# Performance work log

Measured on AMD Instinct MI355X. Metric: run time of the kernel, lower is better.

## Reference

```python
import jax, jax.numpy as jnp
import numpy as np

IN_DIM, OUT_DIM = 256, 64
ALPHA = 0.2  # leaky relu negative slope
NEG_INF = -1e30


def setup_inputs() -> dict:
    key = jax.random.key(0)
    k1, k2, k3, k4 = jax.random.split(key, 4)
    B, N = 8, 2048
    h = jax.random.normal(k1, (B, N, IN_DIM), dtype=jnp.float32)
    adj = jax.random.randint(k2, (B, N, N), 0, 2, dtype=jnp.int32)
    # ensure no fully-isolated node (avoids softmax over all -inf)
    idx = jnp.arange(N)
    adj = adj.at[:, idx, idx].set(1)
    # params: fc.weight [out,in] -> store transposed [in,out]; attn_fc.weight [1, 2*out] -> [2*out]
    W = jax.random.normal(k3, (IN_DIM, OUT_DIM), dtype=jnp.float32) / np.sqrt(IN_DIM)
    a = jax.random.normal(k4, (2 * OUT_DIM,), dtype=jnp.float32) / np.sqrt(2 * OUT_DIM)
    return {"h": h, "adj": adj, "W": W, "a": a}


def reference(h, adj, W, a):
    # Wh: [B,N,D]
    Wh = jnp.einsum("bni,io->bno", h, W)
    D = Wh.shape[-1]
    # concat-based additive attention decomposed: e[b,i,j] = lrelu(a1.Wh_i + a2.Wh_j)
    a1, a2 = a[:D], a[D:]
    s1 = Wh @ a1  # [B,N] contribution of row node i
    s2 = Wh @ a2  # [B,N] contribution of col node j
    e = jax.nn.leaky_relu(s1[:, :, None] + s2[:, None, :], negative_slope=ALPHA)  # [B,N,N]
    e = jnp.where(adj == 0, NEG_INF, e)
    attn = jax.nn.softmax(e, axis=-1)
    # dropout is identity in eval mode
    return jnp.einsum("bij,bjd->bid", attn, Wh)
```

## Files before the change

kernel.cpp:

```cpp
#include <hip/hip_runtime.h>
#include <math.h>

#define NB 8
#define NN 2048
#define IN_DIM 256
#define OUT_DIM 64
#define ALPHA 0.2f
#define JSPLIT 4

typedef __attribute__((ext_vector_type(8))) short bf16x8;
typedef __attribute__((ext_vector_type(4))) float f32x4;
typedef __attribute__((ext_vector_type(4))) int   i32x4;

__device__ __forceinline__ unsigned short f2bf(float x) {
    union { float f; unsigned u; } v; v.f = x;
    unsigned r = v.u + 0x7FFF + ((v.u >> 16) & 1);
    return (unsigned short)(r >> 16);
}

#define WT_STRIDE 264
__global__ __launch_bounds__(256) void wh_kernel(const float* __restrict__ h,
                                                 const float* __restrict__ W,
                                                 const float* __restrict__ a,
                                                 unsigned short* __restrict__ Whbt,
                                                 float* __restrict__ s1,
                                                 float* __restrict__ s2) {
    __shared__ unsigned short Wt[OUT_DIM * WT_STRIDE];
    const int t = threadIdx.x;

    #pragma unroll 8
    for (int rep = 0; rep < 64; ++rep) {
        const int id = rep * 256 + t;
        const int k = id >> 6, n = id & 63;
        Wt[n * WT_STRIDE + k] = f2bf(W[id]);
    }
    __syncthreads();

    const int lane = t & 63, wv = t >> 6;
    const int m = lane & 15, quad = lane >> 4;
    const long gr0 = (long)(blockIdx.x * 4 + wv) * 16;

    f32x4 acc[4];
    #pragma unroll
    for (int nt = 0; nt < 4; ++nt) acc[nt] = (f32x4){0.f, 0.f, 0.f, 0.f};

    #pragma unroll
    for (int ks = 0; ks < 8; ++ks) {
        const int k0 = ks * 32;
        const float* hp = h + (gr0 + m) * IN_DIM + k0 + quad * 8;
        const float4 ha = *(const float4*)hp;
        const float4 hb = *(const float4*)(hp + 4);
        bf16x8 af;
        af[0] = (short)f2bf(ha.x); af[1] = (short)f2bf(ha.y);
        af[2] = (short)f2bf(ha.z); af[3] = (short)f2bf(ha.w);
        af[4] = (short)f2bf(hb.x); af[5] = (short)f2bf(hb.y);
        af[6] = (short)f2bf(hb.z); af[7] = (short)f2bf(hb.w);
        #pragma unroll
        for (int nt = 0; nt < 4; ++nt) {
            const bf16x8 bf_ = *(const bf16x8*)(const void*)
                &Wt[(nt * 16 + m) * WT_STRIDE + k0 + quad * 8];
            acc[nt] = __builtin_amdgcn_mfma_f32_16x16x32_bf16(af, bf_, acc[nt], 0, 0, 0);
        }
    }

    const int b  = (int)(gr0 >> 11);
    const int ib = (int)(gr0 & 2047);

    #pragma unroll
    for (int nt = 0; nt < 4; ++nt) {
        ushort4 w4;
        w4.x = f2bf(acc[nt][0]); w4.y = f2bf(acc[nt][1]);
        w4.z = f2bf(acc[nt][2]); w4.w = f2bf(acc[nt][3]);
        *(ushort4*)&Whbt[((long)(b * OUT_DIM + nt * 16 + m) << 11) + ib + quad * 4] = w4;
    }

    float a1v[4], a2v[4];
    #pragma unroll
    for (int nt = 0; nt < 4; ++nt) {
        a1v[nt] = a[nt * 16 + m];
        a2v[nt] = a[OUT_DIM + nt * 16 + m];
    }
    #pragma unroll
    for (int reg = 0; reg < 4; ++reg) {
        float p1 = 0.f, p2 = 0.f;
        #pragma unroll
        for (int nt = 0; nt < 4; ++nt) {
            p1 += acc[nt][reg] * a1v[nt];
            p2 += acc[nt][reg] * a2v[nt];
        }
        #pragma unroll
        for (int off = 1; off < 16; off <<= 1) {
            p1 += __shfl_xor(p1, off, 64);
            p2 += __shfl_xor(p2, off, 64);
        }
        if (m == 0) {
            s1[gr0 + quad * 4 + reg] = p1;
            s2[gr0 + quad * 4 + reg] = p2;
        }
    }
}

__device__ __forceinline__ float pcalc(int av, float s2e, float s1v) {
    float e = s1v + s2e;
    e = e > 0.f ? e : ALPHA * e;
    const float p = __expf(e);
    return av != 0 ? p : 0.f;
}

__global__ __launch_bounds__(256, 4) void attn_kernel(const int* __restrict__ adj,
                                                      const unsigned short* __restrict__ Whbt,
                                                      const float* __restrict__ s1,
                                                      const float* __restrict__ s2,
                                                      float* __restrict__ part,
                                                      float* __restrict__ lpart) {
    const int t = threadIdx.x, lane = t & 63, wv = t >> 6;
    const int bid = blockIdx.x;
    const int js  = bid & (JSPLIT - 1);
    const int itg = (bid >> 2) & 31;
    const int b   = bid >> 7;
    const int i0  = itg * 64 + wv * 16;
    const int jlo = js * (NN / JSPLIT);

    const int m = lane & 15, quad = lane >> 4;

    const int*   adjp = adj + (long)b * NN * NN + (long)(i0 + m) * NN + jlo + quad * 8;
    const float* s2p  = s2 + b * NN + jlo + quad * 8;
    const unsigned short* wbase = Whbt + ((long)(b * OUT_DIM) << 11) + jlo + quad * 8;
    const float s1v = s1[b * NN + i0 + m];

    f32x4 acc[4];
    #pragma unroll
    for (int nt = 0; nt < 4; ++nt) acc[nt] = (f32x4){0.f, 0.f, 0.f, 0.f};
    f32x4 racc = (f32x4){0.f, 0.f, 0.f, 0.f};

    bf16x8 bones;
    #pragma unroll
    for (int e = 0; e < 8; ++e) bones[e] = (short)0x3F80;

    i32x4  av0[2], av1[2];
    float4 sv0[2], sv1[2];
    #pragma unroll
    for (int p = 0; p < 2; ++p) {
        av0[p] = __builtin_nontemporal_load((const i32x4*)(adjp + p * 32));
        av1[p] = __builtin_nontemporal_load((const i32x4*)(adjp + p * 32 + 4));
        sv0[p] = *(const float4*)(s2p + p * 32);
        sv1[p] = *(const float4*)(s2p + p * 32 + 4);
    }

    #pragma unroll 2
    for (int ks = 0; ks < 16; ++ks) {
        const int j0 = ks * 32;
        const int cur = ks & 1;

        bf16x8 bfr[4];
        #pragma unroll
        for (int nt = 0; nt < 4; ++nt)
            bfr[nt] = *(const bf16x8*)(const void*)
                &wbase[(((long)(nt * 16 + m)) << 11) + j0];

        const i32x4  ca0 = av0[cur], ca1 = av1[cur];
        const float4 cs0 = sv0[cur], cs1 = sv1[cur];
        if (ks < 14) {
            av0[cur] = __builtin_nontemporal_load((const i32x4*)(adjp + j0 + 64));
            av1[cur] = __builtin_nontemporal_load((const i32x4*)(adjp + j0 + 68));
            sv0[cur] = *(const float4*)(s2p + j0 + 64);
            sv1[cur] = *(const float4*)(s2p + j0 + 68);
        }

        float pv[8];
        pv[0] = pcalc(ca0.x, cs0.x, s1v); pv[1] = pcalc(ca0.y, cs0.y, s1v);
        pv[2] = pcalc(ca0.z, cs0.z, s1v); pv[3] = pcalc(ca0.w, cs0.w, s1v);
        pv[4] = pcalc(ca1.x, cs1.x, s1v); pv[5] = pcalc(ca1.y, cs1.y, s1v);
        pv[6] = pcalc(ca1.z, cs1.z, s1v); pv[7] = pcalc(ca1.w, cs1.w, s1v);

        bf16x8 af;
        #pragma unroll
        for (int e = 0; e < 8; ++e) af[e] = (short)f2bf(pv[e]);

        #pragma unroll
        for (int nt = 0; nt < 4; ++nt)
            acc[nt] = __builtin_amdgcn_mfma_f32_16x16x32_bf16(af, bfr[nt], acc[nt], 0, 0, 0);
        racc = __builtin_amdgcn_mfma_f32_16x16x32_bf16(af, bones, racc, 0, 0, 0);
    }

    if (m == 0) {
        #pragma unroll
        for (int reg = 0; reg < 4; ++reg)
            lpart[js * (NB * NN) + b * NN + i0 + quad * 4 + reg] = racc[reg];
    }

    float* pp = part + (long)js * ((long)NB * NN * OUT_DIM)
                     + ((long)(b * NN + i0) << 6);
    #pragma unroll
    for (int nt = 0; nt < 4; ++nt)
        #pragma unroll
        for (int reg = 0; reg < 4; ++reg)
            pp[(quad * 4 + reg) * OUT_DIM + nt * 16 + m] = acc[nt][reg];
}

__global__ __launch_bounds__(256) void finalize_kernel(const float* __restrict__ part,
                                                       const float* __restrict__ lpart,
                                                       float* __restrict__ out) {
    const int idx = blockIdx.x * 256 + threadIdx.x;
    const int row = idx >> 4;
    float l = 0.f;
    #pragma unroll
    for (int s = 0; s < JSPLIT; ++s) l += lpart[s * (NB * NN) + row];
    float4 v = make_float4(0.f, 0.f, 0.f, 0.f);
    const float4* p4 = (const float4*)part;
    #pragma unroll
    for (int s = 0; s < JSPLIT; ++s) {
        const float4 p = p4[(long)s * ((long)NB * NN * OUT_DIM / 4) + idx];
        v.x += p.x; v.y += p.y; v.z += p.z; v.w += p.w;
    }
    const float inv = 1.f / l;
    v.x *= inv; v.y *= inv; v.z *= inv; v.w *= inv;
    ((float4*)out)[idx] = v;
}

extern "C" void kernel_launch(void* const* d_in, const int* in_sizes, int n_in,
                              void* d_out, int out_size, void* d_ws, size_t ws_size,
                              hipStream_t stream) {
    const float* h   = (const float*)d_in[0];
    const int*   adj = (const int*)d_in[1];
    const float* W   = (const float*)d_in[2];
    const float* a   = (const float*)d_in[3];
    float* out = (float*)d_out;

    float* s1    = (float*)d_ws;
    float* s2    = s1 + NB * NN;
    float* lpart = s2 + NB * NN;
    float* part  = lpart + JSPLIT * NB * NN;
    unsigned short* Whbt =
        (unsigned short*)(part + (long)JSPLIT * NB * NN * OUT_DIM);

    wh_kernel<<<NB * NN / 64, 256, 0, stream>>>(h, W, a, Whbt, s1, s2);
    attn_kernel<<<NB * (NN / 64) * JSPLIT, 256, 0, stream>>>(adj, Whbt, s1, s2, part, lpart);
    finalize_kernel<<<NB * NN * OUT_DIM / 4 / 256, 256, 0, stream>>>(part, lpart, out);
}
```

Before: 235.7 us.

## Pack adjacency into bitmask in prep kernel before attention pass

Adds blocks to the projection kernel that compress the int32 adjacency matrix into a 1-bit-per-edge mask. The attention kernel then loads 16 mask words per row up front instead of streaming int32 adjacency with software double-buffering. This separates the bandwidth-heavy adjacency read into a highly parallel simple kernel and shrinks the attention kernel's memory traffic. Total DRAM reads of adj are unchanged, and a small extra write/read of the mask is added.

```diff
diff --git a/kernel.cpp b/kernel.cpp
--- a/kernel.cpp
+++ b/kernel.cpp
@@ -7,6 +7,8 @@
 #define OUT_DIM 64
 #define ALPHA 0.2f
 #define JSPLIT 4
+#define PACK_BLOCKS (NB * NN * NN / 32 / 256)
+#define WH_BLOCKS 256
 
 typedef __attribute__((ext_vector_type(8))) short bf16x8;
 typedef __attribute__((ext_vector_type(4))) float f32x4;
@@ -19,14 +21,33 @@
 }
 
 #define WT_STRIDE 264
-__global__ __launch_bounds__(256) void wh_kernel(const float* __restrict__ h,
-                                                 const float* __restrict__ W,
-                                                 const float* __restrict__ a,
-                                                 unsigned short* __restrict__ Whbt,
-                                                 float* __restrict__ s1,
-                                                 float* __restrict__ s2) {
+__global__ __launch_bounds__(256) void prep_kernel(const float* __restrict__ h,
+                                                   const float* __restrict__ W,
+                                                   const float* __restrict__ a,
+                                                   const int* __restrict__ adj,
+                                                   unsigned* __restrict__ bits,
+                                                   unsigned short* __restrict__ Whbt,
+                                                   float* __restrict__ s1,
+                                                   float* __restrict__ s2) {
     __shared__ unsigned short Wt[OUT_DIM * WT_STRIDE];
     const int t = threadIdx.x;
+    const int bid = blockIdx.x;
+
+    if (bid >= WH_BLOCKS) {
+        const long w = (long)(bid - WH_BLOCKS) * 256 + t;
+        const i32x4* a4 = (const i32x4*)adj + w * 8;
+        unsigned mm = 0;
+        #pragma unroll
+        for (int q = 0; q < 8; ++q) {
+            const i32x4 v = __builtin_nontemporal_load(a4 + q);
+            mm |= (v.x != 0 ? 1u : 0u) << (4 * q);
+            mm |= (v.y != 0 ? 1u : 0u) << (4 * q + 1);
+            mm |= (v.z != 0 ? 1u : 0u) << (4 * q + 2);
+            mm |= (v.w != 0 ? 1u : 0u) << (4 * q + 3);
+        }
+        bits[w] = mm;
+        return;
+    }
 
     #pragma unroll 8
     for (int rep = 0; rep < 64; ++rep) {
@@ -38,7 +59,7 @@
 
     const int lane = t & 63, wv = t >> 6;
     const int m = lane & 15, quad = lane >> 4;
-    const long gr0 = (long)(blockIdx.x * 4 + wv) * 16;
+    const long gr0 = (long)(bid * 4 + wv) * 16;
 
     f32x4 acc[4];
     #pragma unroll
@@ -100,14 +121,14 @@
     }
 }
 
-__device__ __forceinline__ float pcalc(int av, float s2e, float s1v) {
+__device__ __forceinline__ float pcalc(unsigned mask, int bit, float s2e, float s1v) {
     float e = s1v + s2e;
     e = e > 0.f ? e : ALPHA * e;
     const float p = __expf(e);
-    return av != 0 ? p : 0.f;
-}
-
-__global__ __launch_bounds__(256, 4) void attn_kernel(const int* __restrict__ adj,
+    return ((mask >> bit) & 1u) ? p : 0.f;
+}
+
+__global__ __launch_bounds__(256, 4) void attn_kernel(const unsigned* __restrict__ bits,
                                                       const unsigned short* __restrict__ Whbt,
                                                       const float* __restrict__ s1,
                                                       const float* __restrict__ s2,
@@ -123,7 +144,11 @@
 
     const int m = lane & 15, quad = lane >> 4;
 
-    const int*   adjp = adj + (long)b * NN * NN + (long)(i0 + m) * NN + jlo + quad * 8;
+    const i32x4* mp = (const i32x4*)(bits + ((long)(b * NN + i0 + m) << 6) + (jlo >> 5));
+    i32x4 mk[4];
+    #pragma unroll
+    for (int g = 0; g < 4; ++g) mk[g] = mp[g];
+
     const float* s2p  = s2 + b * NN + jlo + quad * 8;
     const unsigned short* wbase = Whbt + ((long)(b * OUT_DIM) << 11) + jlo + quad * 8;
     const float s1v = s1[b * NN + i0 + m];
@@ -137,20 +162,13 @@
     #pragma unroll
     for (int e = 0; e < 8; ++e) bones[e] = (short)0x3F80;
 
-    i32x4  av0[2], av1[2];
-    float4 sv0[2], sv1[2];
-    #pragma unroll
-    for (int p = 0; p < 2; ++p) {
-        av0[p] = __builtin_nontemporal_load((const i32x4*)(adjp + p * 32));
-        av1[p] = __builtin_nontemporal_load((const i32x4*)(adjp + p * 32 + 4));
-        sv0[p] = *(const float4*)(s2p + p * 32);
-        sv1[p] = *(const float4*)(s2p + p * 32 + 4);
-    }
-
-    #pragma unroll 2
+    float4 sv0 = *(const float4*)s2p;
+    float4 sv1 = *(const float4*)(s2p + 4);
+
+    #pragma unroll
     for (int ks = 0; ks < 16; ++ks) {
         const int j0 = ks * 32;
-        const int cur = ks & 1;
+        const unsigned mask = (unsigned)mk[ks >> 2][ks & 3];
 
         bf16x8 bfr[4];
         #pragma unroll
@@ -158,20 +176,22 @@
             bfr[nt] = *(const bf16x8*)(const void*)
                 &wbase[(((long)(nt * 16 + m)) << 11) + j0];
 
-        const i32x4  ca0 = av0[cur], ca1 = av1[cur];
-        const float4 cs0 = sv0[cur], cs1 = sv1[cur];
-        if (ks < 14) {
-            av0[cur] = __builtin_nontemporal_load((const i32x4*)(adjp + j0 + 64));
-            av1[cur] = __builtin_nontemporal_load((const i32x4*)(adjp + j0 + 68));
-            sv0[cur] = *(const float4*)(s2p + j0 + 64);
-            sv1[cur] = *(const float4*)(s2p + j0 + 68);
-        }
-
+        const float4 cs0 = sv0, cs1 = sv1;
+        if (ks < 15) {
+            sv0 = *(const float4*)(s2p + j0 + 32);
+            sv1 = *(const float4*)(s2p + j0 + 36);
+        }
+
+        const int bb = quad * 8;
         float pv[8];
-        pv[0] = pcalc(ca0.x, cs0.x, s1v); pv[1] = pcalc(ca0.y, cs0.y, s1v);
-        pv[2] = pcalc(ca0.z, cs0.z, s1v); pv[3] = pcalc(ca0.w, cs0.w, s1v);
-        pv[4] = pcalc(ca1.x, cs1.x, s1v); pv[5] = pcalc(ca1.y, cs1.y, s1v);
-        pv[6] = pcalc(ca1.z, cs1.z, s1v); pv[7] = pcalc(ca1.w, cs1.w, s1v);
+        pv[0] = pcalc(mask, bb + 0, cs0.x, s1v);
+        pv[1] = pcalc(mask, bb + 1, cs0.y, s1v);
+        pv[2] = pcalc(mask, bb + 2, cs0.z, s1v);
+        pv[3] = pcalc(mask, bb + 3, cs0.w, s1v);
+        pv[4] = pcalc(mask, bb + 4, cs1.x, s1v);
+        pv[5] = pcalc(mask, bb + 5, cs1.y, s1v);
+        pv[6] = pcalc(mask, bb + 6, cs1.z, s1v);
+        pv[7] = pcalc(mask, bb + 7, cs1.w, s1v);
 
         bf16x8 af;
         #pragma unroll
@@ -233,8 +253,11 @@
     float* part  = lpart + JSPLIT * NB * NN;
     unsigned short* Whbt =
         (unsigned short*)(part + (long)JSPLIT * NB * NN * OUT_DIM);
-
-    wh_kernel<<<NB * NN / 64, 256, 0, stream>>>(h, W, a, Whbt, s1, s2);
-    attn_kernel<<<NB * (NN / 64) * JSPLIT, 256, 0, stream>>>(adj, Whbt, s1, s2, part, lpart);
+    unsigned* bits = (unsigned*)(Whbt + (long)NB * NN * OUT_DIM);
+
+    prep_kernel<<<WH_BLOCKS + PACK_BLOCKS, 256, 0, stream>>>(h, W, a, adj, bits,
+                                                             Whbt, s1, s2);
+    attn_kernel<<<NB * (NN / 64) * JSPLIT, 256, 0, stream>>>(bits, Whbt, s1, s2,
+                                                             part, lpart);
     finalize_kernel<<<NB * NN * OUT_DIM / 4 / 256, 256, 0, stream>>>(part, lpart, out);
 }
```

Measured after the change: 269.2 us. +14.2%, slower.
